# Kernel tuning notes

Measured on AMD Instinct MI355X. Metric: run time of the kernel, lower is better.

The kernel has to match this reference:

```python
import jax, jax.numpy as jnp
import numpy as np

N_NODES = 50000
N_EDGES = 800000
D_IN = 128
D_HID = 128
N_CLASSES = 10


def setup_inputs() -> dict:
    key = jax.random.key(0)
    ks = jax.random.split(key, 8)
    x = jax.random.normal(ks[0], (N_NODES, D_IN), dtype=jnp.float32)
    edge_index = jax.random.randint(ks[1], (2, N_EDGES), 0, N_NODES, dtype=jnp.int64)
    s = 1.0 / np.sqrt(D_IN)
    W1 = jax.random.uniform(ks[2], (D_IN, D_HID), jnp.float32, -s, s)
    b1 = jnp.zeros((D_HID,), jnp.float32)
    W2 = jax.random.uniform(ks[3], (D_HID, D_HID), jnp.float32, -s, s)
    b2 = jnp.zeros((D_HID,), jnp.float32)
    sl = 1.0 / np.sqrt(D_HID)
    Wl = jax.random.uniform(ks[4], (D_HID, N_CLASSES), jnp.float32, -sl, sl)
    bl = jax.random.uniform(ks[5], (N_CLASSES,), jnp.float32, -sl, sl)
    return {"x": x, "edge_index": edge_index, "W1": W1, "b1": b1,
            "W2": W2, "b2": b2, "Wl": Wl, "bl": bl}


def gcn_conv(x, src, dst, W, b, n_nodes):
    # PyG GCNConv: add self-loops, symmetric normalization, gather-scatter aggregate
    h = x @ W                                             # [N, D_out]
    loop = jnp.arange(n_nodes, dtype=src.dtype)
    src2 = jnp.concatenate([src, loop])                   # [E+N]
    dst2 = jnp.concatenate([dst, loop])
    deg = jax.ops.segment_sum(jnp.ones_like(dst2, dtype=h.dtype), dst2,
                              num_segments=n_nodes)       # in-degree incl. self-loop
    dinv = jnp.where(deg > 0, jax.lax.rsqrt(deg), 0.0)
    norm = dinv[src2] * dinv[dst2]                        # [E+N]
    msgs = h[src2] * norm[:, None]                        # gather + scale  [E+N, D_out]
    out = jax.ops.segment_sum(msgs, dst2, num_segments=n_nodes)  # scatter-add
    return out + b


def reference(x, edge_index, W1, b1, W2, b2, Wl, bl):
    src, dst = edge_index[0], edge_index[1]
    n = x.shape[0]
    h = jax.nn.relu(gcn_conv(x, src, dst, W1, b1, n))     # dropout is identity in eval
    h = jax.nn.relu(gcn_conv(h, src, dst, W2, b2, n))
    logits = h @ Wl + bl                                  # [N, C]
    return jax.nn.log_softmax(logits, axis=1)
```

## Files before the change

kernel.cpp:

```cpp
#include <hip/hip_runtime.h>
#include <hip/hip_bf16.h>

#define D 128
#define NCLS 10

typedef short bf16x8 __attribute__((ext_vector_type(8)));
typedef float f32x4 __attribute__((ext_vector_type(4)));

static __device__ __forceinline__ float relu(float x){ return fmaxf(x, 0.0f); }
static __device__ __forceinline__ float bf_lo(unsigned v){ return __uint_as_float(v << 16); }
static __device__ __forceinline__ float bf_hi(unsigned v){ return __uint_as_float(v & 0xffff0000u); }
static __device__ __forceinline__ ushort bf16u(float f){
  __hip_bfloat16 h = __float2bfloat16(f);
  return *reinterpret_cast<ushort*>(&h);
}
static __device__ __forceinline__ unsigned relu_bf2(unsigned v){
  if (v & 0x00008000u) v &= 0xFFFF0000u;
  if (v & 0x80000000u) v &= 0x0000FFFFu;
  return v;
}

__global__ __launch_bounds__(256) void k_zero_i32(int* __restrict__ p, int n){
  int i = blockIdx.x*256 + threadIdx.x;
  if (i < n) p[i] = 0;
}

__global__ __launch_bounds__(256) void k_hist(const int* __restrict__ dst,
                                              int* __restrict__ counts, int E){
  int i = blockIdx.x*256 + threadIdx.x;
  if (i < E) atomicAdd(counts + dst[i], 1);
}

__global__ __launch_bounds__(256) void k_scan1(const int* __restrict__ counts,
                                               int* __restrict__ rowPtr,
                                               int* __restrict__ bsum,
                                               float* __restrict__ dinv, int n){
  const int i = blockIdx.x*256 + threadIdx.x;
  const int lane = threadIdx.x & 63;
  const int wid  = threadIdx.x >> 6;
  int v = (i < n) ? counts[i] : 0;
  if (i < n) dinv[i] = rsqrtf((float)(v + 1));
  int s = v;
  #pragma unroll
  for (int off = 1; off < 64; off <<= 1){
    int u = __shfl_up(s, off, 64);
    if (lane >= off) s += u;
  }
  __shared__ int ws[4];
  if (lane == 63) ws[wid] = s;
  __syncthreads();
  int add = 0;
  if (wid >= 1) add += ws[0];
  if (wid >= 2) add += ws[1];
  if (wid >= 3) add += ws[2];
  int incl = s + add;
  if (i < n) rowPtr[i] = incl - v;
  if (threadIdx.x == 255) bsum[blockIdx.x] = incl;
}

__global__ __launch_bounds__(256) void k_scan2(int* __restrict__ bsum,
                                               int* __restrict__ rowPtr,
                                               int nb, int n){
  const int t = threadIdx.x;
  const int lane = t & 63;
  const int wid  = t >> 6;
  int v = (t < nb) ? bsum[t] : 0;
  int s = v;
  #pragma unroll
  for (int off = 1; off < 64; off <<= 1){
    int u = __shfl_up(s, off, 64);
    if (lane >= off) s += u;
  }
  __shared__ int ws[4];
  if (lane == 63) ws[wid] = s;
  __syncthreads();
  int add = 0;
  if (wid >= 1) add += ws[0];
  if (wid >= 2) add += ws[1];
  if (wid >= 3) add += ws[2];
  int incl = s + add;
  if (t < nb) bsum[t] = incl - v;
  if (t == 255) rowPtr[n] = incl;
}

__global__ __launch_bounds__(256) void k_scan3(const int* __restrict__ bsum,
                                               int* __restrict__ rowPtr, int n){
  int i = blockIdx.x*256 + threadIdx.x;
  if (i < n) rowPtr[i] += bsum[blockIdx.x];
}

__global__ __launch_bounds__(256) void k_scatter(const int* __restrict__ src,
                                                 const int* __restrict__ dst,
                                                 const int* __restrict__ rowPtr,
                                                 const float* __restrict__ dinv,
                                                 int* __restrict__ cursor,
                                                 int2* __restrict__ edat, int E){
  int i = blockIdx.x*256 + threadIdx.x;
  if (i >= E) return;
  int d = dst[i];
  int s = src[i];
  int pos = rowPtr[d] + atomicAdd(cursor + d, 1);
  edat[pos] = make_int2(s, __float_as_int(dinv[s]));
}

__global__ __launch_bounds__(256) void k_cvtW(const float* __restrict__ W1,
                                              const float* __restrict__ W2,
                                              ushort* __restrict__ Wt1,
                                              ushort* __restrict__ Wt2){
  int i = blockIdx.x*256 + threadIdx.x;
  int sel = i >> 14;
  int rem = i & 16383;
  int k = rem >> 7, n = rem & 127;
  const float* Ws = sel ? W2 : W1;
  ushort* Wd = sel ? Wt2 : Wt1;
  Wd[n*128 + k] = bf16u(Ws[rem]);
}

template<bool BF16IN, bool RELU>
__global__ __launch_bounds__(256) void k_gemm_mfma(const void* __restrict__ Av,
                                                   const ushort* __restrict__ Wt,
                                                   __hip_bfloat16* __restrict__ C,
                                                   int M){
  __shared__ ushort sA[64*136];
  __shared__ ushort sW[128*136];
  const int tid = threadIdx.x;
  const int row0 = blockIdx.x * 64;
  const int rowsHere = (M - row0 >= 64) ? 64 : (M - row0);

  {
    const uint4* Wt4 = (const uint4*)Wt;
    for (int i = tid; i < 2048; i += 256){
      int r = i >> 4, c = i & 15;
      uint4 v = Wt4[i];
      *((uint4*)(sA + 0, (void)0, sW + r*136 + c*8)) = v;
    }
  }
  if (BF16IN){
    const uint4* A4 = (const uint4*)((const ushort*)Av + (size_t)row0 * D);
    for (int i = tid; i < 64*16; i += 256){
      int r = i >> 4, c = i & 15;
      uint4 v = make_uint4(0,0,0,0);
      if (r < rowsHere) v = A4[i];
      if (RELU){ v.x = relu_bf2(v.x); v.y = relu_bf2(v.y);
                 v.z = relu_bf2(v.z); v.w = relu_bf2(v.w); }
      *((uint4*)(sA + r*136 + c*8)) = v;
    }
  } else {
    const float4* A4 = (const float4*)Av + (size_t)row0 * 32;
    for (int i = tid; i < 64*32; i += 256){
      int r = i >> 5, c = i & 31;
      float4 v = make_float4(0.f,0.f,0.f,0.f);
      if (r < rowsHere) v = A4[i];
      if (RELU){ v.x=relu(v.x); v.y=relu(v.y); v.z=relu(v.z); v.w=relu(v.w); }
      ushort4 p;
      p.x = bf16u(v.x); p.y = bf16u(v.y); p.z = bf16u(v.z); p.w = bf16u(v.w);
      *((ushort4*)(sA + r*136 + c*4)) = p;
    }
  }
  __syncthreads();

  const int wid  = tid >> 6;
  const int lane = tid & 63;
  const int fr = lane & 15;
  const int fq = lane >> 4;
  const ushort* aBase = sA + (wid*16 + fr)*136 + fq*8;
  const ushort* wBase = sW + fr*136 + fq*8;

  f32x4 acc0 = {0.f,0.f,0.f,0.f}, acc1 = acc0, acc2 = acc0, acc3 = acc0;
  f32x4 acc4 = acc0, acc5 = acc0, acc6 = acc0, acc7 = acc0;
  #pragma unroll
  for (int ks = 0; ks < 4; ++ks){
    bf16x8 a = *(const bf16x8*)(aBase + ks*32);
    bf16x8 b;
    b = *(const bf16x8*)(wBase + 0*16*136 + ks*32);
    acc0 = __builtin_amdgcn_mfma_f32_16x16x32_bf16(a, b, acc0, 0, 0, 0);
    b = *(const bf16x8*)(wBase + 1*16*136 + ks*32);
    acc1 = __builtin_amdgcn_mfma_f32_16x16x32_bf16(a, b, acc1, 0, 0, 0);
    b = *(const bf16x8*)(wBase + 2*16*136 + ks*32);
    acc2 = __builtin_amdgcn_mfma_f32_16x16x32_bf16(a, b, acc2, 0, 0, 0);
    b = *(const bf16x8*)(wBase + 3*16*136 + ks*32);
    acc3 = __builtin_amdgcn_mfma_f32_16x16x32_bf16(a, b, acc3, 0, 0, 0);
    b = *(const bf16x8*)(wBase + 4*16*136 + ks*32);
    acc4 = __builtin_amdgcn_mfma_f32_16x16x32_bf16(a, b, acc4, 0, 0, 0);
    b = *(const bf16x8*)(wBase + 5*16*136 + ks*32);
    acc5 = __builtin_amdgcn_mfma_f32_16x16x32_bf16(a, b, acc5, 0, 0, 0);
    b = *(const bf16x8*)(wBase + 6*16*136 + ks*32);
    acc6 = __builtin_amdgcn_mfma_f32_16x16x32_bf16(a, b, acc6, 0, 0, 0);
    b = *(const bf16x8*)(wBase + 7*16*136 + ks*32);
    acc7 = __builtin_amdgcn_mfma_f32_16x16x32_bf16(a, b, acc7, 0, 0, 0);
  }

  const int rbase = row0 + wid*16 + fq*4;
  #pragma unroll
  for (int r = 0; r < 4; ++r){
    int row = rbase + r;
    if (row < M){
      __hip_bfloat16* crow = C + (size_t)row*D + fr;
      crow[0*16]  = __float2bfloat16(acc0[r]);
      crow[1*16]  = __float2bfloat16(acc1[r]);
      crow[2*16]  = __float2bfloat16(acc2[r]);
      crow[3*16]  = __float2bfloat16(acc3[r]);
      crow[4*16]  = __float2bfloat16(acc4[r]);
      crow[5*16]  = __float2bfloat16(acc5[r]);
      crow[6*16]  = __float2bfloat16(acc6[r]);
      crow[7*16]  = __float2bfloat16(acc7[r]);
    }
  }
}

#define AGG_CORE_BF16                                                          \
  const int grp = lane >> 4;                                                   \
  const int q   = lane & 15;                                                   \
  float dn = dinv[node];                                                       \
  float4 aA0 = make_float4(0,0,0,0), aB0 = aA0, aA1 = aA0, aB1 = aA0;          \
  int beg = rowPtr[node], end = rowPtr[node+1];                                \
  for (int j = beg; j < end; j += 64){                                         \
    int rem = end - j;                                                         \
    int cnt = (rem < 64) ? rem : 64;                                           \
    int2 ed = make_int2(0, 0);                                                 \
    if (lane < cnt) ed = edat[j + lane];                                       \
    int T = (((cnt + 3) >> 2) + 1) & ~1;                                       \
    for (int t = 0; t < T; t += 2){                                            \
      _Pragma("unroll")                                                        \
      for (int u = 0; u < 2; ++u){                                             \
        int e = 4*(t+u) + grp;                                                 \
        int sb = __shfl(ed.x, e);                                              \
        float nb = __uint_as_float((unsigned)__shfl(ed.y, e)) * dn;            \
        uint4 hv = ((const uint4*)(h + (size_t)sb*D))[q];                      \
        float4& cA = u ? aA1 : aA0;                                            \
        float4& cB = u ? aB1 : aB0;                                            \
        cA.x += bf_lo(hv.x)*nb; cA.y += bf_hi(hv.x)*nb;                        \
        cA.z += bf_lo(hv.y)*nb; cA.w += bf_hi(hv.y)*nb;                        \
        cB.x += bf_lo(hv.z)*nb; cB.y += bf_hi(hv.z)*nb;                        \
        cB.z += bf_lo(hv.w)*nb; cB.w += bf_hi(hv.w)*nb;                        \
      }                                                                        \
    }                                                                          \
  }                                                                            \
  float4 rA, rB;                                                               \
  rA.x=aA0.x+aA1.x; rA.y=aA0.y+aA1.y; rA.z=aA0.z+aA1.z; rA.w=aA0.w+aA1.w;      \
  rB.x=aB0.x+aB1.x; rB.y=aB0.y+aB1.y; rB.z=aB0.z+aB1.z; rB.w=aB0.w+aB1.w;      \
  rA.x += __shfl_xor(rA.x,16,64); rA.y += __shfl_xor(rA.y,16,64);              \
  rA.z += __shfl_xor(rA.z,16,64); rA.w += __shfl_xor(rA.w,16,64);              \
  rB.x += __shfl_xor(rB.x,16,64); rB.y += __shfl_xor(rB.y,16,64);              \
  rB.z += __shfl_xor(rB.z,16,64); rB.w += __shfl_xor(rB.w,16,64);              \
  rA.x += __shfl_xor(rA.x,32,64); rA.y += __shfl_xor(rA.y,32,64);              \
  rA.z += __shfl_xor(rA.z,32,64); rA.w += __shfl_xor(rA.w,32,64);              \
  rB.x += __shfl_xor(rB.x,32,64); rB.y += __shfl_xor(rB.y,32,64);              \
  rB.z += __shfl_xor(rB.z,32,64); rB.w += __shfl_xor(rB.w,32,64);

__global__ __launch_bounds__(256) void k_agg_csr(const ushort* __restrict__ h,
                                                 const int* __restrict__ rowPtr,
                                                 const int2* __restrict__ edat,
                                                 const float* __restrict__ dinv,
                                                 const float* __restrict__ b,
                                                 ushort* __restrict__ out, int n){
  int gid = blockIdx.x*256 + threadIdx.x;
  int node = gid >> 6;
  int lane = gid & 63;
  if (node >= n) return;
  AGG_CORE_BF16
  if (grp != 0) return;
  uint4 hs = ((const uint4*)(h + (size_t)node*D))[q];
  float sl = dn * dn;
  float4 bA = ((const float4*)b)[2*q];
  float4 bB = ((const float4*)b)[2*q + 1];
  float r[8];
  r[0] = rA.x + bf_lo(hs.x)*sl + bA.x;
  r[1] = rA.y + bf_hi(hs.x)*sl + bA.y;
  r[2] = rA.z + bf_lo(hs.y)*sl + bA.z;
  r[3] = rA.w + bf_hi(hs.y)*sl + bA.w;
  r[4] = rB.x + bf_lo(hs.z)*sl + bB.x;
  r[5] = rB.y + bf_hi(hs.z)*sl + bB.y;
  r[6] = rB.z + bf_lo(hs.w)*sl + bB.z;
  r[7] = rB.w + bf_hi(hs.w)*sl + bB.w;
  union Pack { uint4 u; __hip_bfloat16 b[8]; } p;
  #pragma unroll
  for (int i = 0; i < 8; ++i) p.b[i] = __float2bfloat16(r[i]);
  ((uint4*)(out + (size_t)node*D))[q] = p.u;
}

__global__ __launch_bounds__(256) void k_agg_head(const ushort* __restrict__ h,
                                                  const int* __restrict__ rowPtr,
                                                  const int2* __restrict__ edat,
                                                  const float* __restrict__ dinv,
                                                  const float* __restrict__ b,
                                                  const float* __restrict__ Wl,
                                                  const float* __restrict__ bl,
                                                  float* __restrict__ out, int n){
  int gid = blockIdx.x*256 + threadIdx.x;
  int node = gid >> 6;
  int lane = gid & 63;
  if (node >= n) return;
  AGG_CORE_BF16
  if (grp != 0) return;
  uint4 hs = ((const uint4*)(h + (size_t)node*D))[q];
  float sl = dn * dn;
  float4 bA = ((const float4*)b)[2*q];
  float4 bB = ((const float4*)b)[2*q + 1];
  float r[8];
  r[0] = relu(rA.x + bf_lo(hs.x)*sl + bA.x);
  r[1] = relu(rA.y + bf_hi(hs.x)*sl + bA.y);
  r[2] = relu(rA.z + bf_lo(hs.y)*sl + bA.z);
  r[3] = relu(rA.w + bf_hi(hs.y)*sl + bA.w);
  r[4] = relu(rB.x + bf_lo(hs.z)*sl + bB.x);
  r[5] = relu(rB.y + bf_hi(hs.z)*sl + bB.y);
  r[6] = relu(rB.z + bf_lo(hs.w)*sl + bB.z);
  r[7] = relu(rB.w + bf_hi(hs.w)*sl + bB.w);
  float lacc[NCLS];
  #pragma unroll
  for (int c = 0; c < NCLS; ++c){
    float a = 0.f;
    #pragma unroll
    for (int i = 0; i < 8; ++i) a += r[i] * Wl[(8*q + i)*NCLS + c];
    lacc[c] = a;
  }
  #pragma unroll
  for (int c = 0; c < NCLS; ++c){
    #pragma unroll
    for (int off = 8; off >= 1; off >>= 1)
      lacc[c] += __shfl_xor(lacc[c], off, 16);
    lacc[c] += bl[c];
  }
  float m = lacc[0];
  #pragma unroll
  for (int c = 1; c < NCLS; ++c) m = fmaxf(m, lacc[c]);
  float se = 0.f;
  #pragma unroll
  for (int c = 0; c < NCLS; ++c) se += expf(lacc[c] - m);
  float lse = m + logf(se);
  if (q < NCLS){
    float v = lacc[0];
    #pragma unroll
    for (int c = 1; c < NCLS; ++c) if (q == c) v = lacc[c];
    out[(size_t)node*NCLS + q] = v - lse;
  }
}

extern "C" void kernel_launch(void* const* d_in, const int* in_sizes, int n_in,
                              void* d_out, int out_size, void* d_ws, size_t ws_size,
                              hipStream_t stream){
  const float* x  = (const float*)d_in[0];
  const int*   ei = (const int*)d_in[1];
  const float* W1 = (const float*)d_in[2];
  const float* b1 = (const float*)d_in[3];
  const float* W2 = (const float*)d_in[4];
  const float* b2 = (const float*)d_in[5];
  const float* Wl = (const float*)d_in[6];
  const float* bl = (const float*)d_in[7];
  float* out = (float*)d_out;

  const int N = in_sizes[0] / D;
  const int E = in_sizes[1] / 2;
  const int* src = ei;
  const int* dst = ei + E;

  char* ws = (char*)d_ws;
  size_t off = 0;
  ushort* h1    = (ushort*)(ws + off); off += (size_t)N*D*2;
  ushort* g1    = (ushort*)(ws + off); off += (size_t)N*D*2;
  ushort* h2    = (ushort*)(ws + off); off += (size_t)N*D*2;
  ushort* Wt1   = (ushort*)(ws + off); off += (size_t)128*128*2;
  ushort* Wt2   = (ushort*)(ws + off); off += (size_t)128*128*2;
  int*   counts = (int*)(ws + off);    off += (size_t)N*4;
  int*   cursor = (int*)(ws + off);    off += (size_t)N*4;
  int*   rowPtr = (int*)(ws + off);    off += (size_t)(N+2)*4;
  float* dinv   = (float*)(ws + off);  off += (size_t)N*4;
  int*   bsum   = (int*)(ws + off);    off += (size_t)256*4;
  int2*  edat   = (int2*)(ws + off);   off += (size_t)E*8;

  const int nbN   = (N + 255)/256;
  const int nb2N  = (2*N + 255)/256;
  const int nbE   = (E + 255)/256;
  const int gemmB = (N + 63)/64;
  const int aggB  = (N + 3)/4;

  k_zero_i32<<<nb2N, 256, 0, stream>>>(counts, 2*N);
  k_hist<<<nbE, 256, 0, stream>>>(dst, counts, E);
  k_scan1<<<nbN, 256, 0, stream>>>(counts, rowPtr, bsum, dinv, N);
  k_scan2<<<1, 256, 0, stream>>>(bsum, rowPtr, nbN, N);
  k_scan3<<<nbN, 256, 0, stream>>>(bsum, rowPtr, N);
  k_scatter<<<nbE, 256, 0, stream>>>(src, dst, rowPtr, dinv, cursor, edat, E);
  k_cvtW<<<128, 256, 0, stream>>>(W1, W2, Wt1, Wt2);

  k_gemm_mfma<false,false><<<gemmB, 256, 0, stream>>>(x, Wt1, (__hip_bfloat16*)h1, N);
  k_agg_csr<<<aggB, 256, 0, stream>>>(h1, rowPtr, edat, dinv, b1, g1, N);

  k_gemm_mfma<true,true><<<gemmB, 256, 0, stream>>>(g1, Wt2, (__hip_bfloat16*)h2, N);
  k_agg_head<<<aggB, 256, 0, stream>>>(h2, rowPtr, edat, dinv, b2, Wl, bl, out, N);
}
```

Measured before the change: 211.0 us.

## Split hidden features into column blocks for cache-resident gather aggregation

```diff
diff --git a/kernel.cpp b/kernel.cpp
--- a/kernel.cpp
+++ b/kernel.cpp
@@ -3,6 +3,8 @@
 
 #define D 128
 #define NCLS 10
+#define FB 32
+#define NBLK 4
 
 typedef short bf16x8 __attribute__((ext_vector_type(8)));
 typedef float f32x4 __attribute__((ext_vector_type(4)));
@@ -119,7 +121,7 @@
 template<bool BF16IN, bool RELU>
 __global__ __launch_bounds__(256) void k_gemm_mfma(const void* __restrict__ Av,
                                                    const ushort* __restrict__ Wt,
-                                                   __hip_bfloat16* __restrict__ C,
+                                                   ushort* __restrict__ C,
                                                    int M){
   __shared__ ushort sA[64*136];
   __shared__ ushort sW[128*136];
@@ -132,15 +134,16 @@
     for (int i = tid; i < 2048; i += 256){
       int r = i >> 4, c = i & 15;
       uint4 v = Wt4[i];
-      *((uint4*)(sA + 0, (void)0, sW + r*136 + c*8)) = v;
+      *((uint4*)(sW + r*136 + c*8)) = v;
     }
   }
   if (BF16IN){
-    const uint4* A4 = (const uint4*)((const ushort*)Av + (size_t)row0 * D);
+    const ushort* Ab = (const ushort*)Av;
     for (int i = tid; i < 64*16; i += 256){
       int r = i >> 4, c = i & 15;
       uint4 v = make_uint4(0,0,0,0);
-      if (r < rowsHere) v = A4[i];
+      if (r < rowsHere)
+        v = *(const uint4*)(Ab + ((size_t)(c>>2)*M + row0 + r)*FB + (c&3)*8);
       if (RELU){ v.x = relu_bf2(v.x); v.y = relu_bf2(v.y);
                  v.z = relu_bf2(v.z); v.w = relu_bf2(v.w); }
       *((uint4*)(sA + r*136 + c*8)) = v;
@@ -195,145 +198,144 @@
   for (int r = 0; r < 4; ++r){
     int row = rbase + r;
     if (row < M){
-      __hip_bfloat16* crow = C + (size_t)row*D + fr;
-      crow[0*16]  = __float2bfloat16(acc0[r]);
-      crow[1*16]  = __float2bfloat16(acc1[r]);
-      crow[2*16]  = __float2bfloat16(acc2[r]);
-      crow[3*16]  = __float2bfloat16(acc3[r]);
-      crow[4*16]  = __float2bfloat16(acc4[r]);
-      crow[5*16]  = __float2bfloat16(acc5[r]);
-      crow[6*16]  = __float2bfloat16(acc6[r]);
-      crow[7*16]  = __float2bfloat16(acc7[r]);
+      #define STORE_BLK(j, accv) \
+        C[((size_t)((j)>>1)*M + row)*FB + ((j)&1)*16 + fr] = bf16u((accv)[r]);
+      STORE_BLK(0, acc0) STORE_BLK(1, acc1) STORE_BLK(2, acc2) STORE_BLK(3, acc3)
+      STORE_BLK(4, acc4) STORE_BLK(5, acc5) STORE_BLK(6, acc6) STORE_BLK(7, acc7)
+      #undef STORE_BLK
     }
   }
 }
 
-#define AGG_CORE_BF16                                                          \
-  const int grp = lane >> 4;                                                   \
-  const int q   = lane & 15;                                                   \
+#define AGG_CORE_BLK                                                           \
+  const int grp = lane >> 3;                                                   \
+  const int q   = lane & 7;                                                    \
   float dn = dinv[node];                                                       \
-  float4 aA0 = make_float4(0,0,0,0), aB0 = aA0, aA1 = aA0, aB1 = aA0;          \
+  float4 a0 = make_float4(0,0,0,0), a1 = a0;                                   \
   int beg = rowPtr[node], end = rowPtr[node+1];                                \
   for (int j = beg; j < end; j += 64){                                         \
     int rem = end - j;                                                         \
     int cnt = (rem < 64) ? rem : 64;                                           \
     int2 ed = make_int2(0, 0);                                                 \
     if (lane < cnt) ed = edat[j + lane];                                       \
-    int T = (((cnt + 3) >> 2) + 1) & ~1;                                       \
-    for (int t = 0; t < T; t += 2){                                            \
-      _Pragma("unroll")                                                        \
-      for (int u = 0; u < 2; ++u){                                             \
-        int e = 4*(t+u) + grp;                                                 \
-        int sb = __shfl(ed.x, e);                                              \
-        float nb = __uint_as_float((unsigned)__shfl(ed.y, e)) * dn;            \
-        uint4 hv = ((const uint4*)(h + (size_t)sb*D))[q];                      \
-        float4& cA = u ? aA1 : aA0;                                            \
-        float4& cB = u ? aB1 : aB0;                                            \
-        cA.x += bf_lo(hv.x)*nb; cA.y += bf_hi(hv.x)*nb;                        \
-        cA.z += bf_lo(hv.y)*nb; cA.w += bf_hi(hv.y)*nb;                        \
-        cB.x += bf_lo(hv.z)*nb; cB.y += bf_hi(hv.z)*nb;                        \
-        cB.z += bf_lo(hv.w)*nb; cB.w += bf_hi(hv.w)*nb;                        \
-      }                                                                        \
+    int T = (cnt + 15) >> 4;                                                   \
+    for (int t = 0; t < T; ++t){                                               \
+      int e0 = 16*t + grp;                                                     \
+      int e1 = 16*t + 8 + grp;                                                 \
+      int   sb0 = __shfl(ed.x, e0, 64);                                        \
+      float nb0 = __uint_as_float((unsigned)__shfl(ed.y, e0, 64)) * dn;        \
+      int   sb1 = __shfl(ed.x, e1, 64);                                        \
+      float nb1 = __uint_as_float((unsigned)__shfl(ed.y, e1, 64)) * dn;        \
+      uint2 hv0 = *(const uint2*)(hB + (size_t)sb0*FB + q*4);                  \
+      uint2 hv1 = *(const uint2*)(hB + (size_t)sb1*FB + q*4);                  \
+      a0.x += bf_lo(hv0.x)*nb0; a0.y += bf_hi(hv0.x)*nb0;                      \
+      a0.z += bf_lo(hv0.y)*nb0; a0.w += bf_hi(hv0.y)*nb0;                      \
+      a1.x += bf_lo(hv1.x)*nb1; a1.y += bf_hi(hv1.x)*nb1;                      \
+      a1.z += bf_lo(hv1.y)*nb1; a1.w += bf_hi(hv1.y)*nb1;                      \
     }                                                                          \
   }                                                                            \
-  float4 rA, rB;                                                               \
-  rA.x=aA0.x+aA1.x; rA.y=aA0.y+aA1.y; rA.z=aA0.z+aA1.z; rA.w=aA0.w+aA1.w;      \
-  rB.x=aB0.x+aB1.x; rB.y=aB0.y+aB1.y; rB.z=aB0.z+aB1.z; rB.w=aB0.w+aB1.w;      \
-  rA.x += __shfl_xor(rA.x,16,64); rA.y += __shfl_xor(rA.y,16,64);              \
-  rA.z += __shfl_xor(rA.z,16,64); rA.w += __shfl_xor(rA.w,16,64);              \
-  rB.x += __shfl_xor(rB.x,16,64); rB.y += __shfl_xor(rB.y,16,64);              \
-  rB.z += __shfl_xor(rB.z,16,64); rB.w += __shfl_xor(rB.w,16,64);              \
-  rA.x += __shfl_xor(rA.x,32,64); rA.y += __shfl_xor(rA.y,32,64);              \
-  rA.z += __shfl_xor(rA.z,32,64); rA.w += __shfl_xor(rA.w,32,64);              \
-  rB.x += __shfl_xor(rB.x,32,64); rB.y += __shfl_xor(rB.y,32,64);              \
-  rB.z += __shfl_xor(rB.z,32,64); rB.w += __shfl_xor(rB.w,32,64);
-
-__global__ __launch_bounds__(256) void k_agg_csr(const ushort* __restrict__ h,
-                                                 const int* __restrict__ rowPtr,
-                                                 const int2* __restrict__ edat,
-                                                 const float* __restrict__ dinv,
-                                                 const float* __restrict__ b,
-                                                 ushort* __restrict__ out, int n){
-  int gid = blockIdx.x*256 + threadIdx.x;
-  int node = gid >> 6;
-  int lane = gid & 63;
+  float4 rr;                                                                   \
+  rr.x = a0.x + a1.x; rr.y = a0.y + a1.y;                                      \
+  rr.z = a0.z + a1.z; rr.w = a0.w + a1.w;                                      \
+  rr.x += __shfl_xor(rr.x, 8, 64); rr.y += __shfl_xor(rr.y, 8, 64);            \
+  rr.z += __shfl_xor(rr.z, 8, 64); rr.w += __shfl_xor(rr.w, 8, 64);            \
+  rr.x += __shfl_xor(rr.x,16, 64); rr.y += __shfl_xor(rr.y,16, 64);            \
+  rr.z += __shfl_xor(rr.z,16, 64); rr.w += __shfl_xor(rr.w,16, 64);            \
+  rr.x += __shfl_xor(rr.x,32, 64); rr.y += __shfl_xor(rr.y,32, 64);            \
+  rr.z += __shfl_xor(rr.z,32, 64); rr.w += __shfl_xor(rr.w,32, 64);
+
+__global__ __launch_bounds__(256) void k_agg1_blk(const ushort* __restrict__ h,
+                                                  const int* __restrict__ rowPtr,
+                                                  const int2* __restrict__ edat,
+                                                  const float* __restrict__ dinv,
+                                                  const float* __restrict__ b,
+                                                  ushort* __restrict__ out,
+                                                  int n, int nodeBlocks){
+  const int phase = blockIdx.x / nodeBlocks;
+  const int nb_   = blockIdx.x % nodeBlocks;
+  const int node  = nb_*4 + (threadIdx.x >> 6);
+  const int lane  = threadIdx.x & 63;
   if (node >= n) return;
-  AGG_CORE_BF16
+  const ushort* hB = h + (size_t)phase*n*FB;
+  AGG_CORE_BLK
   if (grp != 0) return;
-  uint4 hs = ((const uint4*)(h + (size_t)node*D))[q];
+  uint2 hs = *(const uint2*)(hB + (size_t)node*FB + q*4);
   float sl = dn * dn;
-  float4 bA = ((const float4*)b)[2*q];
-  float4 bB = ((const float4*)b)[2*q + 1];
-  float r[8];
-  r[0] = rA.x + bf_lo(hs.x)*sl + bA.x;
-  r[1] = rA.y + bf_hi(hs.x)*sl + bA.y;
-  r[2] = rA.z + bf_lo(hs.y)*sl + bA.z;
-  r[3] = rA.w + bf_hi(hs.y)*sl + bA.w;
-  r[4] = rB.x + bf_lo(hs.z)*sl + bB.x;
-  r[5] = rB.y + bf_hi(hs.z)*sl + bB.y;
-  r[6] = rB.z + bf_lo(hs.w)*sl + bB.z;
-  r[7] = rB.w + bf_hi(hs.w)*sl + bB.w;
-  union Pack { uint4 u; __hip_bfloat16 b[8]; } p;
-  #pragma unroll
-  for (int i = 0; i < 8; ++i) p.b[i] = __float2bfloat16(r[i]);
-  ((uint4*)(out + (size_t)node*D))[q] = p.u;
-}
-
-__global__ __launch_bounds__(256) void k_agg_head(const ushort* __restrict__ h,
+  float4 bv = ((const float4*)b)[phase*8 + q];
+  float r0 = rr.x + bf_lo(hs.x)*sl + bv.x;
+  float r1 = rr.y + bf_hi(hs.x)*sl + bv.y;
+  float r2 = rr.z + bf_lo(hs.y)*sl + bv.z;
+  float r3 = rr.w + bf_hi(hs.y)*sl + bv.w;
+  union { uint2 u; ushort s[4]; } p;
+  p.s[0] = bf16u(r0); p.s[1] = bf16u(r1); p.s[2] = bf16u(r2); p.s[3] = bf16u(r3);
+  *(uint2*)(out + (size_t)phase*n*FB + (size_t)node*FB + q*4) = p.u;
+}
+
+__global__ __launch_bounds__(256) void k_agg2_blk(const ushort* __restrict__ h,
                                                   const int* __restrict__ rowPtr,
                                                   const int2* __restrict__ edat,
                                                   const float* __restrict__ dinv,
                                                   const float* __restrict__ b,
                                                   const float* __restrict__ Wl,
-                                                  const float* __restrict__ bl,
-                                                  float* __restrict__ out, int n){
-  int gid = blockIdx.x*256 + threadIdx.x;
-  int node = gid >> 6;
-  int lane = gid & 63;
+                                                  float* __restrict__ plog,
+                                                  int n, int nodeBlocks){
+  const int phase = blockIdx.x / nodeBlocks;
+  const int nb_   = blockIdx.x % nodeBlocks;
+  const int node  = nb_*4 + (threadIdx.x >> 6);
+  const int lane  = threadIdx.x & 63;
   if (node >= n) return;
-  AGG_CORE_BF16
-  if (grp != 0) return;
-  uint4 hs = ((const uint4*)(h + (size_t)node*D))[q];
+  const ushort* hB = h + (size_t)phase*n*FB;
+  AGG_CORE_BLK
+  uint2 hs = *(const uint2*)(hB + (size_t)node*FB + q*4);
   float sl = dn * dn;
-  float4 bA = ((const float4*)b)[2*q];
-  float4 bB = ((const float4*)b)[2*q + 1];
-  float r[8];
-  r[0] = relu(rA.x + bf_lo(hs.x)*sl + bA.x);
-  r[1] = relu(rA.y + bf_hi(hs.x)*sl + bA.y);
-  r[2] = relu(rA.z + bf_lo(hs.y)*sl + bA.z);
-  r[3] = relu(rA.w + bf_hi(hs.y)*sl + bA.w);
-  r[4] = relu(rB.x + bf_lo(hs.z)*sl + bB.x);
-  r[5] = relu(rB.y + bf_hi(hs.z)*sl + bB.y);
-  r[6] = relu(rB.z + bf_lo(hs.w)*sl + bB.z);
-  r[7] = relu(rB.w + bf_hi(hs.w)*sl + bB.w);
+  float4 bv = ((const float4*)b)[phase*8 + q];
+  float r[4];
+  r[0] = relu(rr.x + bf_lo(hs.x)*sl + bv.x);
+  r[1] = relu(rr.y + bf_hi(hs.x)*sl + bv.y);
+  r[2] = relu(rr.z + bf_lo(hs.y)*sl + bv.z);
+  r[3] = relu(rr.w + bf_hi(hs.y)*sl + bv.w);
+  const int f0 = phase*FB + q*4;
   float lacc[NCLS];
   #pragma unroll
   for (int c = 0; c < NCLS; ++c){
-    float a = 0.f;
-    #pragma unroll
-    for (int i = 0; i < 8; ++i) a += r[i] * Wl[(8*q + i)*NCLS + c];
-    lacc[c] = a;
+    lacc[c] = r[0]*Wl[(f0+0)*NCLS + c] + r[1]*Wl[(f0+1)*NCLS + c]
+            + r[2]*Wl[(f0+2)*NCLS + c] + r[3]*Wl[(f0+3)*NCLS + c];
   }
   #pragma unroll
   for (int c = 0; c < NCLS; ++c){
-    #pragma unroll
-    for (int off = 8; off >= 1; off >>= 1)
-      lacc[c] += __shfl_xor(lacc[c], off, 16);
-    lacc[c] += bl[c];
-  }
-  float m = lacc[0];
-  #pragma unroll
-  for (int c = 1; c < NCLS; ++c) m = fmaxf(m, lacc[c]);
-  float se = 0.f;
-  #pragma unroll
-  for (int c = 0; c < NCLS; ++c) se += expf(lacc[c] - m);
-  float lse = m + logf(se);
-  if (q < NCLS){
+    lacc[c] += __shfl_xor(lacc[c], 1, 64);
+    lacc[c] += __shfl_xor(lacc[c], 2, 64);
+    lacc[c] += __shfl_xor(lacc[c], 4, 64);
+  }
+  if (lane < NCLS){
     float v = lacc[0];
     #pragma unroll
-    for (int c = 1; c < NCLS; ++c) if (q == c) v = lacc[c];
-    out[(size_t)node*NCLS + q] = v - lse;
-  }
+    for (int c = 1; c < NCLS; ++c) if (lane == c) v = lacc[c];
+    plog[((size_t)phase*n + node)*NCLS + lane] = v;
+  }
+}
+
+__global__ __launch_bounds__(256) void k_head_final(const float* __restrict__ plog,
+                                                    const float* __restrict__ bl,
+                                                    float* __restrict__ out, int n){
+  int node = blockIdx.x*256 + threadIdx.x;
+  if (node >= n) return;
+  float l[NCLS];
+  #pragma unroll
+  for (int c = 0; c < NCLS; ++c)
+    l[c] = plog[(size_t)node*NCLS + c]
+         + plog[((size_t)n + node)*NCLS + c]
+         + plog[((size_t)2*n + node)*NCLS + c]
+         + plog[((size_t)3*n + node)*NCLS + c] + bl[c];
+  float m = l[0];
+  #pragma unroll
+  for (int c = 1; c < NCLS; ++c) m = fmaxf(m, l[c]);
+  float se = 0.f;
+  #pragma unroll
+  for (int c = 0; c < NCLS; ++c) se += expf(l[c] - m);
+  float lse = m + logf(se);
+  #pragma unroll
+  for (int c = 0; c < NCLS; ++c) out[(size_t)node*NCLS + c] = l[c] - lse;
 }
 
 extern "C" void kernel_launch(void* const* d_in, const int* in_sizes, int n_in,
@@ -366,13 +368,15 @@
   int*   rowPtr = (int*)(ws + off);    off += (size_t)(N+2)*4;
   float* dinv   = (float*)(ws + off);  off += (size_t)N*4;
   int*   bsum   = (int*)(ws + off);    off += (size_t)256*4;
+  float* plog   = (float*)(ws + off);  off += (size_t)NBLK*N*NCLS*4;
   int2*  edat   = (int2*)(ws + off);   off += (size_t)E*8;
 
   const int nbN   = (N + 255)/256;
   const int nb2N  = (2*N + 255)/256;
   const int nbE   = (E + 255)/256;
   const int gemmB = (N + 63)/64;
-  const int aggB  = (N + 3)/4;
+  const int nodeBlocks = (N + 3)/4;
+  const int aggB  = NBLK * nodeBlocks;
 
   k_zero_i32<<<nb2N, 256, 0, stream>>>(counts, 2*N);
   k_hist<<<nbE, 256, 0, stream>>>(dst, counts, E);
@@ -382,9 +386,10 @@
   k_scatter<<<nbE, 256, 0, stream>>>(src, dst, rowPtr, dinv, cursor, edat, E);
   k_cvtW<<<128, 256, 0, stream>>>(W1, W2, Wt1, Wt2);
 
-  k_gemm_mfma<false,false><<<gemmB, 256, 0, stream>>>(x, Wt1, (__hip_bfloat16*)h1, N);
-  k_agg_csr<<<aggB, 256, 0, stream>>>(h1, rowPtr, edat, dinv, b1, g1, N);
-
-  k_gemm_mfma<true,true><<<gemmB, 256, 0, stream>>>(g1, Wt2, (__hip_bfloat16*)h2, N);
-  k_agg_head<<<aggB, 256, 0, stream>>>(h2, rowPtr, edat, dinv, b2, Wl, bl, out, N);
-}
+  k_gemm_mfma<false,false><<<gemmB, 256, 0, stream>>>(x, Wt1, h1, N);
+  k_agg1_blk<<<aggB, 256, 0, stream>>>(h1, rowPtr, edat, dinv, b1, g1, N, nodeBlocks);
+
+  k_gemm_mfma<true,true><<<gemmB, 256, 0, stream>>>(g1, Wt2, h2, N);
+  k_agg2_blk<<<aggB, 256, 0, stream>>>(h2, rowPtr, edat, dinv, b2, Wl, plog, N, nodeBlocks);
+  k_head_final<<<nbN, 256, 0, stream>>>(plog, bl, out, N);
+}
```

Result: slower. 332.2 us (+57.5%).
